# Kernel tuning notes

Measured on AMD Instinct MI355X. Metric: run time of the kernel, lower is better.

## Reference

```python
import jax, jax.numpy as jnp
import numpy as np

K = 10
ALPHA = 0.1
BETA = 0.9
GAMMA = BETA ** K + ALPHA * sum(BETA ** i for i in range(K))


def setup_inputs() -> dict:
    key = jax.random.key(0)
    k1, k2, k3 = jax.random.split(key, 3)
    N, D, E = 100000, 256, 1600000
    x = jax.random.normal(k1, (N, D), dtype=jnp.float32)
    edge_weight = jax.random.uniform(k2, (E,), dtype=jnp.float32)
    edge_index = jax.random.randint(k3, (2, E), 0, N, dtype=jnp.int32)
    return {"x": x, "edge_weight": edge_weight, "edge_index": edge_index}


def reference(x, edge_weight, edge_index):
    N = x.shape[0]
    # gcn_norm_adj with renorm: add self-loops (weight 1) then D^-1/2 A D^-1/2
    loops = jnp.arange(N, dtype=edge_index.dtype)
    row = jnp.concatenate([edge_index[0], loops])
    col = jnp.concatenate([edge_index[1], loops])
    w = jnp.concatenate([edge_weight, jnp.ones((N,), dtype=x.dtype)])
    deg = jax.ops.segment_sum(w, row, num_segments=N)
    dinv = jnp.where(deg > 0, jax.lax.rsqrt(deg), 0.0)
    wn = dinv[row] * w * dinv[col]  # normalized edge weights [E+N]

    h = x
    out = h
    for _ in range(K):
        # SpMM: out[r] = sum_e wn[e] * out[col[e]] for row[e]==r
        msg = wn[:, None] * out[col]
        out = jax.ops.segment_sum(msg, row, num_segments=N)
        out = out * BETA + h * ALPHA
    out = out / GAMMA
    return out
```

## Files before the change

### kernel.cpp

```cpp
#include <hip/hip_runtime.h>
#include <hip/hip_fp16.h>
#include <math.h>

#define DFEAT 256
#define KITER 10
#define ALPHA 0.1f
#define BETA 0.9f


__global__ void count_deg_kernel(const int* __restrict__ row,
                                 const float* __restrict__ w,
                                 float* __restrict__ deg,
                                 int* __restrict__ counts, int E) {
    int e = blockIdx.x * 256 + threadIdx.x;
    if (e < E) {
        int r = row[e];
        atomicAdd(&deg[r], w[e]);
        atomicAdd(&counts[r], 1);
    }
}

__global__ void dinv_kernel(float* __restrict__ deg, int n) {
    int i = blockIdx.x * 256 + threadIdx.x;
    if (i < n) deg[i] = rsqrtf(deg[i] + 1.0f);
}

__global__ void scan_kernel(const int* __restrict__ counts,
                            int* __restrict__ row_ptr,
                            int* __restrict__ fill, int n) {
    __shared__ int tmp[1024];
    int tid = threadIdx.x;
    int carry = 0;
    for (int base = 0; base < n; base += 1024) {
        int i = base + tid;
        int v = (i < n) ? counts[i] : 0;
        tmp[tid] = v;
        __syncthreads();
        for (int off = 1; off < 1024; off <<= 1) {
            int t = (tid >= off) ? tmp[tid - off] : 0;
            __syncthreads();
            tmp[tid] += t;
            __syncthreads();
        }
        int incl = tmp[tid];
        int excl = incl - v + carry;
        if (i < n) { row_ptr[i] = excl; fill[i] = excl; }
        int total = tmp[1023];
        __syncthreads();
        carry += total;
    }
    if (tid == 0) row_ptr[n] = carry;
}

__global__ void scatter_kernel(const int* __restrict__ row, const int* __restrict__ col,
                               const float* __restrict__ w, const float* __restrict__ dinv,
                               int* __restrict__ fill, int2* __restrict__ cw, int E) {
    int e = blockIdx.x * 256 + threadIdx.x;
    if (e < E) {
        int r = row[e], c = col[e];
        float wn = dinv[r] * w[e] * dinv[c];
        int pos = atomicAdd(&fill[r], 1);
        cw[pos] = make_int2(c, __float_as_int(wn));
    }
}

__global__ void f2h_kernel(const float* __restrict__ src, __half* __restrict__ dst,
                           size_t n4) {
    size_t i = (size_t)blockIdx.x * 256 + threadIdx.x;
    if (i < n4) {
        float4 v = ((const float4*)src)[i];
        __half2 h0 = __floats2half2_rn(v.x, v.y);
        __half2 h1 = __floats2half2_rn(v.z, v.w);
        float2 o;
        o.x = *reinterpret_cast<float*>(&h0);
        o.y = *reinterpret_cast<float*>(&h1);
        ((float2*)dst)[i] = o;
    }
}

#define ACC(g, wbits) { float wv = __int_as_float(wbits); \
    __half2 h0_ = *reinterpret_cast<__half2*>(&g.x); \
    __half2 h1_ = *reinterpret_cast<__half2*>(&g.y); \
    float2 u0_ = __half22float2(h0_); float2 u1_ = __half22float2(h1_); \
    a0 += wv * u0_.x; a1 += wv * u0_.y; a2 += wv * u1_.x; a3 += wv * u1_.y; }

template<int FINAL>
__global__ __launch_bounds__(256) void spmm_h_kernel(
        const __half* __restrict__ in, const __half* __restrict__ xh,
        float* __restrict__ outf, __half* __restrict__ outh,
        const int* __restrict__ row_ptr, const int2* __restrict__ cw,
        const float* __restrict__ dinv,
        int n, float scale) {
    int wave = threadIdx.x >> 6;
    int lane = threadIdx.x & 63;
    int r = blockIdx.x * 4 + wave;
    if (r >= n) return;

    int start = row_ptr[r];
    int end   = row_ptr[r + 1];
    float dr  = dinv[r];
    float ws  = dr * dr;

    float2 xraw = ((const float2*)(xh + (size_t)r * DFEAT))[lane];

    float2 sraw = ((const float2*)(in + (size_t)r * DFEAT))[lane];
    __half2 s0 = *reinterpret_cast<__half2*>(&sraw.x);
    __half2 s1 = *reinterpret_cast<__half2*>(&sraw.y);
    float2 sf0 = __half22float2(s0), sf1 = __half22float2(s1);
    float a0 = ws * sf0.x, a1 = ws * sf0.y, a2 = ws * sf1.x, a3 = ws * sf1.y;

    int e = start;
    for (; e + 4 <= end; e += 4) {
        int2 p0 = cw[e];
        int2 p1 = cw[e + 1];
        int2 p2 = cw[e + 2];
        int2 p3 = cw[e + 3];
        float2 g0 = ((const float2*)(in + (size_t)p0.x * DFEAT))[lane];
        float2 g1 = ((const float2*)(in + (size_t)p1.x * DFEAT))[lane];
        float2 g2 = ((const float2*)(in + (size_t)p2.x * DFEAT))[lane];
        float2 g3 = ((const float2*)(in + (size_t)p3.x * DFEAT))[lane];
        ACC(g0, p0.y);
        ACC(g1, p1.y);
        ACC(g2, p2.y);
        ACC(g3, p3.y);
    }
    for (; e < end; ++e) {
        int2 p = cw[e];
        float2 g = ((const float2*)(in + (size_t)p.x * DFEAT))[lane];
        ACC(g, p.y);
    }

    __half2 x0 = *reinterpret_cast<__half2*>(&xraw.x);
    __half2 x1 = *reinterpret_cast<__half2*>(&xraw.y);
    float2 xf0 = __half22float2(x0), xf1 = __half22float2(x1);
    float o0 = scale * (BETA * a0 + ALPHA * xf0.x);
    float o1 = scale * (BETA * a1 + ALPHA * xf0.y);
    float o2 = scale * (BETA * a2 + ALPHA * xf1.x);
    float o3 = scale * (BETA * a3 + ALPHA * xf1.y);

    if (FINAL) {
        ((float4*)(outf + (size_t)r * DFEAT))[lane] = make_float4(o0, o1, o2, o3);
    } else {
        __half2 h0 = __floats2half2_rn(o0, o1);
        __half2 h1 = __floats2half2_rn(o2, o3);
        float2 o;
        o.x = *reinterpret_cast<float*>(&h0);
        o.y = *reinterpret_cast<float*>(&h1);
        ((float2*)(outh + (size_t)r * DFEAT))[lane] = o;
    }
}


extern "C" void kernel_launch(void* const* d_in, const int* in_sizes, int n_in,
                              void* d_out, int out_size, void* d_ws, size_t ws_size,
                              hipStream_t stream) {
    const float* x  = (const float*)d_in[0];
    const float* ew = (const float*)d_in[1];
    const int*   ei = (const int*)d_in[2];
    int n = in_sizes[0] / DFEAT;
    int E = in_sizes[1];
    const int* row = ei;
    const int* col = ei + E;
    float* out = (float*)d_out;

    char* ws = (char*)d_ws;
    auto alloc = [&](size_t bytes) {
        char* p = ws;
        ws += (bytes + 255) & ~(size_t)255;
        return p;
    };
    float*  deg     = (float*)alloc((size_t)n * 4);
    int*    counts  = (int*)  alloc((size_t)n * 4);
    int*    row_ptr = (int*)  alloc((size_t)(n + 1) * 4);
    int*    fill    = (int*)  alloc((size_t)n * 4);
    int2*   cw      = (int2*) alloc((size_t)E * 8);
    __half* xh      = (__half*)alloc((size_t)n * DFEAT * 2);
    __half* H0      = (__half*)alloc((size_t)n * DFEAT * 2);
    __half* H1      = (__half*)d_out;

    hipMemsetAsync(deg, 0, (size_t)n * 4, stream);
    hipMemsetAsync(counts, 0, (size_t)n * 4, stream);

    count_deg_kernel<<<(E + 255) / 256, 256, 0, stream>>>(row, ew, deg, counts, E);
    dinv_kernel<<<(n + 255) / 256, 256, 0, stream>>>(deg, n);
    scan_kernel<<<1, 1024, 0, stream>>>(counts, row_ptr, fill, n);
    scatter_kernel<<<(E + 255) / 256, 256, 0, stream>>>(row, col, ew, deg, fill, cw, E);

    size_t n4 = (size_t)n * DFEAT / 4;
    f2h_kernel<<<(int)((n4 + 255) / 256), 256, 0, stream>>>(x, xh, n4);

    double gamma = pow((double)BETA, KITER);
    for (int i = 0; i < KITER; ++i) gamma += (double)ALPHA * pow((double)BETA, i);
    float inv_gamma = (float)(1.0 / gamma);

    int grid = (n + 3) / 4;
    const __half* cur = xh;
    __half* bufs[2] = { H0, H1 };
    for (int k = 0; k < KITER; ++k) {
        if (k < KITER - 1) {
            __half* o = bufs[k & 1];
            spmm_h_kernel<0><<<grid, 256, 0, stream>>>(cur, xh, nullptr, o,
                                                       row_ptr, cw, deg, n, 1.0f);
            cur = o;
        } else {
            spmm_h_kernel<1><<<grid, 256, 0, stream>>>(cur, xh, out, nullptr,
                                                       row_ptr, cw, deg, n, inv_gamma);
        }
    }
}
```

Baseline: 1.701 ms.

## Replace single-block serial prefix scan with three-phase multi-block scan

The single-block 1024-thread scan over all row counts is replaced by a three-pass scan. Each block scans a 2048-element chunk using wave shuffles, a single block scans the per-chunk totals, and a final pass adds the chunk offsets and writes the fill array. This removes a serial loop of about 100 iterations, each with many block barriers, from the CSR build, at the cost of two extra kernel launches. The scan of chunk totals assumes at most 1024 chunks, and the last row_ptr entry is set to E directly.

```diff
diff --git a/kernel.cpp b/kernel.cpp
--- a/kernel.cpp
+++ b/kernel.cpp
@@ -6,6 +6,7 @@
 #define KITER 10
 #define ALPHA 0.1f
 #define BETA 0.9f
+#define SCAN_CHUNK 2048
 
 
 __global__ void count_deg_kernel(const int* __restrict__ row,
@@ -25,31 +26,69 @@
     if (i < n) deg[i] = rsqrtf(deg[i] + 1.0f);
 }
 
-__global__ void scan_kernel(const int* __restrict__ counts,
-                            int* __restrict__ row_ptr,
-                            int* __restrict__ fill, int n) {
+
+__global__ __launch_bounds__(256) void scan1_kernel(const int* __restrict__ counts,
+                                                    int* __restrict__ row_ptr,
+                                                    int* __restrict__ partial, int n) {
+    __shared__ int wsum[4];
+    int b = blockIdx.x;
+    int base = b * SCAN_CHUNK;
+    int tid = threadIdx.x;
+    int lane = tid & 63, wv = tid >> 6;
+
+    int v[8];
+    int s = 0;
+    #pragma unroll
+    for (int j = 0; j < 8; ++j) {
+        int i = base + tid * 8 + j;
+        v[j] = (i < n) ? counts[i] : 0;
+        s += v[j];
+    }
+    int incl = s;
+    #pragma unroll
+    for (int off = 1; off < 64; off <<= 1) {
+        int t = __shfl_up(incl, off, 64);
+        if (lane >= off) incl += t;
+    }
+    if (lane == 63) wsum[wv] = incl;
+    __syncthreads();
+    int woff = 0;
+    for (int w = 0; w < wv; ++w) woff += wsum[w];
+    int run = woff + incl - s;
+    #pragma unroll
+    for (int j = 0; j < 8; ++j) {
+        int i = base + tid * 8 + j;
+        if (i < n) row_ptr[i] = run;
+        run += v[j];
+    }
+    if (tid == 255) partial[b] = run;
+}
+
+__global__ void scan2_kernel(int* __restrict__ partial, int nb) {
     __shared__ int tmp[1024];
     int tid = threadIdx.x;
-    int carry = 0;
-    for (int base = 0; base < n; base += 1024) {
-        int i = base + tid;
-        int v = (i < n) ? counts[i] : 0;
-        tmp[tid] = v;
+    int v = (tid < nb) ? partial[tid] : 0;
+    tmp[tid] = v;
+    __syncthreads();
+    for (int off = 1; off < 1024; off <<= 1) {
+        int t = (tid >= off) ? tmp[tid - off] : 0;
         __syncthreads();
-        for (int off = 1; off < 1024; off <<= 1) {
-            int t = (tid >= off) ? tmp[tid - off] : 0;
-            __syncthreads();
-            tmp[tid] += t;
-            __syncthreads();
-        }
-        int incl = tmp[tid];
-        int excl = incl - v + carry;
-        if (i < n) { row_ptr[i] = excl; fill[i] = excl; }
-        int total = tmp[1023];
+        tmp[tid] += t;
         __syncthreads();
-        carry += total;
-    }
-    if (tid == 0) row_ptr[n] = carry;
+    }
+    if (tid < nb) partial[tid] = tmp[tid] - v;
+}
+
+__global__ void scan3_kernel(int* __restrict__ row_ptr, int* __restrict__ fill,
+                             const int* __restrict__ partial, int n, int E) {
+    int i = blockIdx.x * 256 + threadIdx.x;
+    if (i < n) {
+        int v = row_ptr[i] + partial[i / SCAN_CHUNK];
+        row_ptr[i] = v;
+        fill[i] = v;
+    } else if (i == n) {
+        row_ptr[n] = E;
+    }
 }
 
 __global__ void scatter_kernel(const int* __restrict__ row, const int* __restrict__ col,
@@ -173,6 +212,7 @@
     int*    counts  = (int*)  alloc((size_t)n * 4);
     int*    row_ptr = (int*)  alloc((size_t)(n + 1) * 4);
     int*    fill    = (int*)  alloc((size_t)n * 4);
+    int*    partial = (int*)  alloc((size_t)1024 * 4);
     int2*   cw      = (int2*) alloc((size_t)E * 8);
     __half* xh      = (__half*)alloc((size_t)n * DFEAT * 2);
     __half* H0      = (__half*)alloc((size_t)n * DFEAT * 2);
@@ -183,7 +223,12 @@
 
     count_deg_kernel<<<(E + 255) / 256, 256, 0, stream>>>(row, ew, deg, counts, E);
     dinv_kernel<<<(n + 255) / 256, 256, 0, stream>>>(deg, n);
-    scan_kernel<<<1, 1024, 0, stream>>>(counts, row_ptr, fill, n);
+
+    int nb = (n + SCAN_CHUNK - 1) / SCAN_CHUNK;
+    scan1_kernel<<<nb, 256, 0, stream>>>(counts, row_ptr, partial, n);
+    scan2_kernel<<<1, 1024, 0, stream>>>(partial, nb);
+    scan3_kernel<<<(n + 256) / 256, 256, 0, stream>>>(row_ptr, fill, partial, n, E);
+
     scatter_kernel<<<(E + 255) / 256, 256, 0, stream>>>(row, col, ew, deg, fill, cw, E);
 
     size_t n4 = (size_t)n * DFEAT / 4;
```

Result: faster. 1.555 ms (-8.6%).
